# Performance work log

Hardware: AMD Instinct MI355X
Metric: run time of the kernel (lower is better)

Reference implementation:

```python
import jax, jax.numpy as jnp
from jax import lax
import numpy as np

LATENT = 64
NUM_LAYERS = 16
HIDDEN = 16
BATCH = 262144
NEG_SLOPE = 0.01


def setup_inputs() -> dict:
    key = jax.random.key(0)
    ks = jax.random.split(key, 9)
    scale = 0.1
    return {
        "x": jax.random.normal(ks[0], (BATCH, LATENT), dtype=jnp.float32),
        "sW1": scale * jax.random.normal(ks[1], (NUM_LAYERS, HIDDEN, LATENT), dtype=jnp.float32),
        "sb1": scale * jax.random.normal(ks[2], (NUM_LAYERS, HIDDEN), dtype=jnp.float32),
        "sW2": scale * jax.random.normal(ks[3], (NUM_LAYERS, LATENT, HIDDEN), dtype=jnp.float32),
        "sb2": scale * jax.random.normal(ks[4], (NUM_LAYERS, LATENT), dtype=jnp.float32),
        "tW1": scale * jax.random.normal(ks[5], (NUM_LAYERS, HIDDEN, LATENT), dtype=jnp.float32),
        "tb1": scale * jax.random.normal(ks[6], (NUM_LAYERS, HIDDEN), dtype=jnp.float32),
        "tW2": scale * jax.random.normal(ks[7], (NUM_LAYERS, LATENT, HIDDEN), dtype=jnp.float32),
        "tb2": scale * jax.random.normal(ks[8], (NUM_LAYERS, LATENT), dtype=jnp.float32),
    }


def _realnvp_forward(x, sW1, sb1, sW2, sb2, tW1, tb1, tW2, tb2):
    L, d = sW1.shape[0], x.shape[-1]
    # b[i] = 1 - i % 2  -> 1 on even indices; even layers use b, odd layers use 1-b
    base = (jnp.arange(d) % 2 == 0).astype(x.dtype)
    layer_even = (jnp.arange(L) % 2 == 0)[:, None]
    masks = jnp.where(layer_even, base[None, :], 1.0 - base[None, :])  # [L, d]

    def step(carry, p):
        z, ld = carry
        W1s, b1s, W2s, b2s, W1t, b1t, W2t, b2t, m = p
        zm = z * m  # [B, d]
        # s-net: Linear -> LeakyReLU(0.01) -> Linear -> Tanh
        hs = jax.nn.leaky_relu(zm @ W1s.T + b1s, NEG_SLOPE)
        scale = jnp.tanh(hs @ W2s.T + b2s)
        # t-net: Linear -> LeakyReLU(0.01) -> Linear
        ht = jax.nn.leaky_relu(zm @ W1t.T + b1t, NEG_SLOPE)
        trans = ht @ W2t.T + b2t
        # MaskedAffineFlow: z' = b*z + (1-b)*(z*exp(s) + t)
        z = zm + (1.0 - m) * (z * jnp.exp(scale) + trans)
        ld = ld + jnp.sum((1.0 - m) * scale, axis=-1)
        return (z, ld), None

    init = (x, jnp.zeros(x.shape[0], dtype=x.dtype))
    (z, ld), _ = lax.scan(step, init, (sW1, sb1, sW2, sb2, tW1, tb1, tW2, tb2, masks))
    return z[..., None], ld


def reference(x, sW1, sb1, sW2, sb2, tW1, tb1, tW2, tb2):
    return _realnvp_forward(x, sW1, sb1, sW2, sb2, tW1, tb1, tW2, tb2)
```

## Files before the change

kernel.cpp:

```cpp
#include <hip/hip_runtime.h>
#include <hip/hip_bf16.h>

#define NL 16
#define HID 16
#define LAT 64
#define BATCHN 262144

typedef __attribute__((ext_vector_type(4))) float f32x4;
typedef __attribute__((ext_vector_type(8))) short b16x8;

__device__ __forceinline__ f32x4 MFMA32(b16x8 a, b16x8 b, f32x4 c) {
  return __builtin_amdgcn_mfma_f32_16x16x32_bf16(a, b, c, 0, 0, 0);
}

__device__ __forceinline__ unsigned pk2(float lo, float hi) {
  __hip_bfloat162 h2 = __float22bfloat162_rn(float2{lo, hi});
  union { __hip_bfloat162 h; unsigned u; } u; u.h = h2; return u.u;
}

#if __has_builtin(__builtin_amdgcn_exp2f)
__device__ __forceinline__ float fexp2(float x) { return __builtin_amdgcn_exp2f(x); }
#else
__device__ __forceinline__ float fexp2(float x) { return __expf(0.6931471805599453f * x); }
#endif
#if __has_builtin(__builtin_amdgcn_rcpf)
__device__ __forceinline__ float frcp(float x) { return __builtin_amdgcn_rcpf(x); }
#else
__device__ __forceinline__ float frcp(float x) { return __fdividef(1.f, x); }
#endif

__device__ __forceinline__ short bfs(float f) {
  union { __hip_bfloat16 h; short s; } u; u.h = __float2bfloat16(f); return u.s;
}
__device__ __forceinline__ float leaky(float v) { return fmaxf(v, 0.01f * v); }
#define TWO_LOG2E 2.885390081777927f
#define LOG2E     1.442695040888963f

__global__ void prep_frags(
    const float* __restrict__ sW1, const float* __restrict__ sb1,
    const float* __restrict__ sW2, const float* __restrict__ sb2,
    const float* __restrict__ tW1, const float* __restrict__ tb1,
    const float* __restrict__ tW2, const float* __restrict__ tb2,
    b16x8* __restrict__ A1S, b16x8* __restrict__ A1T,
    b16x8* __restrict__ A2S, b16x8* __restrict__ A2T,
    f32x4* __restrict__ B1S, f32x4* __restrict__ B1T,
    f32x4* __restrict__ C2S, f32x4* __restrict__ C2T)
{
  const int l = blockIdx.x;
  const int lane = threadIdx.x;
  const int c = lane & 15, g = lane >> 4;
  const int PR = l & 1, PW = 1 - PR;
  const int idx = l * 64 + lane;

  b16x8 a;
  const float* w = sW1 + (l * HID + c) * LAT;
#pragma unroll
  for (int u = 0; u < 8; ++u) a[u] = bfs(w[16 * g + 2 * u + PR]);
  A1S[idx] = a;
  w = tW1 + (l * HID + c) * LAT;
#pragma unroll
  for (int u = 0; u < 8; ++u) a[u] = bfs(w[16 * g + 2 * u + PR]);
  A1T[idx] = a;
  B1S[idx] = ((const f32x4*)(sb1 + l * HID))[g];
  B1T[idx] = ((const f32x4*)(tb1 + l * HID))[g];

#pragma unroll
  for (int to = 0; to < 2; ++to) {
    const int m = 8 * (c >> 2) + 4 * to + (c & 3);
    const int d = 2 * m + PW;
    const int i2 = (l * 2 + to) * 64 + lane;
    b16x8 as = {0, 0, 0, 0, 0, 0, 0, 0}, at = {0, 0, 0, 0, 0, 0, 0, 0};
    const float* w2 = sW2 + (l * LAT + d) * HID + 4 * g;
#pragma unroll
    for (int j = 0; j < 4; ++j) as[j] = bfs(w2[j]);
    w2 = tW2 + (l * LAT + d) * HID + 4 * g;
#pragma unroll
    for (int j = 0; j < 4; ++j) at[4 + j] = bfs(w2[j]);
    A2S[i2] = as;
    A2T[i2] = at;
    f32x4 cs, ct;
#pragma unroll
    for (int j = 0; j < 4; ++j) {
      cs[j] = sb2[l * LAT + 16 * g + 8 * to + 2 * j + PW];
      ct[j] = tb2[l * LAT + 16 * g + 8 * to + 2 * j + PW];
    }
    C2S[i2] = cs;
    C2T[i2] = ct;
  }
}

template<int PR>
__device__ __forceinline__ void layer_step(
    b16x8 a1s, b16x8 a1t, b16x8 a2s0, b16x8 a2s1, b16x8 a2t0, b16x8 a2t1,
    f32x4 b1sv, f32x4 b1tv, f32x4 c2s0, f32x4 c2s1, f32x4 c2t0, f32x4 c2t1,
    f32x4 (&zst)[2][2][2], b16x8 (&zbf)[2][2], float (&rsum)[2][2])
{
  constexpr int PW = 1 - PR;
#pragma unroll
  for (int T = 0; T < 2; ++T) {
    const f32x4 hs = MFMA32(a1s, zbf[T][PR], b1sv);
    const f32x4 ht = MFMA32(a1t, zbf[T][PR], b1tv);
    union { unsigned u[4]; b16x8 v; } hc;
    hc.u[0] = pk2(leaky(hs[0]), leaky(hs[1]));
    hc.u[1] = pk2(leaky(hs[2]), leaky(hs[3]));
    hc.u[2] = pk2(leaky(ht[0]), leaky(ht[1]));
    hc.u[3] = pk2(leaky(ht[2]), leaky(ht[3]));
    const f32x4 ds0 = MFMA32(a2s0, hc.v, c2s0);
    const f32x4 dt0 = MFMA32(a2t0, hc.v, c2t0);
    const f32x4 ds1 = MFMA32(a2s1, hc.v, c2s1);
    const f32x4 dt1 = MFMA32(a2t1, hc.v, c2t1);
    f32x4 z0 = zst[T][PW][0], z1 = zst[T][PW][1];
#pragma unroll
    for (int j = 0; j < 4; ++j) {
      const float w0 = fexp2(TWO_LOG2E * ds0[j]);
      const float r0 = frcp(w0 + 1.f);
      rsum[T][0] += r0;
      z0[j] = fmaf(z0[j], fexp2(fmaf(-TWO_LOG2E, r0, LOG2E)), dt0[j]);
      const float w1 = fexp2(TWO_LOG2E * ds1[j]);
      const float r1 = frcp(w1 + 1.f);
      rsum[T][1] += r1;
      z1[j] = fmaf(z1[j], fexp2(fmaf(-TWO_LOG2E, r1, LOG2E)), dt1[j]);
    }
    zst[T][PW][0] = z0;
    zst[T][PW][1] = z1;
    union { unsigned u[4]; b16x8 v; } nz;
    nz.u[0] = pk2(z0[0], z0[1]);
    nz.u[1] = pk2(z0[2], z0[3]);
    nz.u[2] = pk2(z1[0], z1[1]);
    nz.u[3] = pk2(z1[2], z1[3]);
    zbf[T][PW] = nz.v;
  }
}

__global__ __launch_bounds__(256) void realnvp_fwd(
    const float* __restrict__ x, float* __restrict__ out,
    const b16x8* __restrict__ A1S, const b16x8* __restrict__ A1T,
    const b16x8* __restrict__ A2S, const b16x8* __restrict__ A2T,
    const f32x4* __restrict__ B1S, const f32x4* __restrict__ B1T,
    const f32x4* __restrict__ C2S, const f32x4* __restrict__ C2T)
{
  const int lane = threadIdx.x & 63;
  const int wv = threadIdx.x >> 6;
  const int c = lane & 15, g = lane >> 4;
  const int rowbase = (blockIdx.x * 4 + wv) * 32;

  f32x4 zst[2][2][2];
  b16x8 zbf[2][2];
  float rsum[2][2] = {{0.f, 0.f}, {0.f, 0.f}};
#pragma unroll
  for (int T = 0; T < 2; ++T) {
    const f32x4* xr = (const f32x4*)(x + (size_t)(rowbase + T * 16 + c) * LAT);
    const f32x4 q0 = xr[4 * g], q1 = xr[4 * g + 1], q2 = xr[4 * g + 2], q3 = xr[4 * g + 3];
    zst[T][0][0] = (f32x4){q0[0], q0[2], q1[0], q1[2]};
    zst[T][1][0] = (f32x4){q0[1], q0[3], q1[1], q1[3]};
    zst[T][0][1] = (f32x4){q2[0], q2[2], q3[0], q3[2]};
    zst[T][1][1] = (f32x4){q2[1], q2[3], q3[1], q3[3]};
#pragma unroll
    for (int p = 0; p < 2; ++p) {
      union { unsigned u[4]; b16x8 v; } zb;
      zb.u[0] = pk2(zst[T][p][0][0], zst[T][p][0][1]);
      zb.u[1] = pk2(zst[T][p][0][2], zst[T][p][0][3]);
      zb.u[2] = pk2(zst[T][p][1][0], zst[T][p][1][1]);
      zb.u[3] = pk2(zst[T][p][1][2], zst[T][p][1][3]);
      zbf[T][p] = zb.v;
    }
  }

#pragma unroll 2
  for (int lp = 0; lp < NL / 2; ++lp) {
    {
      const int i1 = (2 * lp) * 64 + lane, i2 = (4 * lp) * 64 + lane;
      layer_step<0>(A1S[i1], A1T[i1], A2S[i2], A2S[i2 + 64], A2T[i2], A2T[i2 + 64],
                    B1S[i1], B1T[i1], C2S[i2], C2S[i2 + 64], C2T[i2], C2T[i2 + 64],
                    zst, zbf, rsum);
    }
    {
      const int i1 = (2 * lp + 1) * 64 + lane, i2 = (4 * lp + 2) * 64 + lane;
      layer_step<1>(A1S[i1], A1T[i1], A2S[i2], A2S[i2 + 64], A2T[i2], A2T[i2 + 64],
                    B1S[i1], B1T[i1], C2S[i2], C2S[i2 + 64], C2T[i2], C2T[i2 + 64],
                    zst, zbf, rsum);
    }
  }

#pragma unroll
  for (int T = 0; T < 2; ++T) {
    f32x4* zo = (f32x4*)(out + (size_t)(rowbase + T * 16 + c) * LAT);
    const f32x4 e0 = zst[T][0][0], o0 = zst[T][1][0];
    const f32x4 e1 = zst[T][0][1], o1 = zst[T][1][1];
    zo[4 * g]     = (f32x4){e0[0], o0[0], e0[1], o0[1]};
    zo[4 * g + 1] = (f32x4){e0[2], o0[2], e0[3], o0[3]};
    zo[4 * g + 2] = (f32x4){e1[0], o1[0], e1[1], o1[1]};
    zo[4 * g + 3] = (f32x4){e1[2], o1[2], e1[3], o1[3]};
  }
  float ldv[2];
#pragma unroll
  for (int T = 0; T < 2; ++T) {
    float rs = rsum[T][0] + rsum[T][1];
    rs += __shfl_xor(rs, 16, 64);
    rs += __shfl_xor(rs, 32, 64);
    ldv[T] = fmaf(-2.f, rs, 512.f);
  }
  if (g < 2)
    out[(size_t)BATCHN * LAT + rowbase + g * 16 + c] = g ? ldv[1] : ldv[0];
}

extern "C" void kernel_launch(void* const* d_in, const int* in_sizes, int n_in,
                              void* d_out, int out_size, void* d_ws, size_t ws_size,
                              hipStream_t stream) {
  const float* x   = (const float*)d_in[0];
  const float* sW1 = (const float*)d_in[1];
  const float* sb1 = (const float*)d_in[2];
  const float* sW2 = (const float*)d_in[3];
  const float* sb2 = (const float*)d_in[4];
  const float* tW1 = (const float*)d_in[5];
  const float* tb1 = (const float*)d_in[6];
  const float* tW2 = (const float*)d_in[7];
  const float* tb2 = (const float*)d_in[8];
  float* out = (float*)d_out;

  char* w = (char*)d_ws;
  b16x8* A1S = (b16x8*)w;            w += NL * 64 * sizeof(b16x8);
  b16x8* A1T = (b16x8*)w;            w += NL * 64 * sizeof(b16x8);
  b16x8* A2S = (b16x8*)w;            w += NL * 128 * sizeof(b16x8);
  b16x8* A2T = (b16x8*)w;            w += NL * 128 * sizeof(b16x8);
  f32x4* B1S = (f32x4*)w;            w += NL * 64 * sizeof(f32x4);
  f32x4* B1T = (f32x4*)w;            w += NL * 64 * sizeof(f32x4);
  f32x4* C2S = (f32x4*)w;            w += NL * 128 * sizeof(f32x4);
  f32x4* C2T = (f32x4*)w;            w += NL * 128 * sizeof(f32x4);

  hipLaunchKernelGGL(prep_frags, dim3(NL), dim3(64), 0, stream,
                     sW1, sb1, sW2, sb2, tW1, tb1, tW2, tb2,
                     A1S, A1T, A2S, A2T, B1S, B1T, C2S, C2T);
  hipLaunchKernelGGL(realnvp_fwd, dim3(BATCHN / 128), dim3(256), 0, stream,
                     x, out, A1S, A1T, A2S, A2T, B1S, B1T, C2S, C2T);
}
```

Measured before the change: 105.1 us.

## Interleave per-layer weight fragments, fold tanh scale into weights, batch reciprocals

Prep now writes all fragments for one layer into a contiguous 12 KB block with a single base pointer, and pre-multiplies the s-net second layer weights and bias by 2*log2e so the exp2 argument needs no scaling. The tanh step replaces four reciprocals with one shared reciprocal of the product of four terms, with a clamp to avoid overflow. The main kernel moves to 64-thread blocks, one wave each, and the layer loop is no longer unrolled. This cuts transcendental and address work, at the cost of extra multiplies, possible precision loss from the product reciprocal, and four times as many blocks.

New measurement: 114.7 us. 1.09x slower.

```diff
diff --git a/kernel.cpp b/kernel.cpp
--- a/kernel.cpp
+++ b/kernel.cpp
@@ -5,6 +5,7 @@
 #define HID 16
 #define LAT 64
 #define BATCHN 262144
+#define LSTRIDE 12288
 
 typedef __attribute__((ext_vector_type(4))) float f32x4;
 typedef __attribute__((ext_vector_type(8))) short b16x8;
@@ -41,65 +42,75 @@
     const float* __restrict__ sW2, const float* __restrict__ sb2,
     const float* __restrict__ tW1, const float* __restrict__ tb1,
     const float* __restrict__ tW2, const float* __restrict__ tb2,
-    b16x8* __restrict__ A1S, b16x8* __restrict__ A1T,
-    b16x8* __restrict__ A2S, b16x8* __restrict__ A2T,
-    f32x4* __restrict__ B1S, f32x4* __restrict__ B1T,
-    f32x4* __restrict__ C2S, f32x4* __restrict__ C2T)
+    char* __restrict__ ws)
 {
   const int l = blockIdx.x;
   const int lane = threadIdx.x;
   const int c = lane & 15, g = lane >> 4;
   const int PR = l & 1, PW = 1 - PR;
-  const int idx = l * 64 + lane;
+  char* base = ws + (size_t)l * LSTRIDE + lane * 16;
 
   b16x8 a;
   const float* w = sW1 + (l * HID + c) * LAT;
 #pragma unroll
   for (int u = 0; u < 8; ++u) a[u] = bfs(w[16 * g + 2 * u + PR]);
-  A1S[idx] = a;
+  *(b16x8*)(base) = a;
   w = tW1 + (l * HID + c) * LAT;
 #pragma unroll
   for (int u = 0; u < 8; ++u) a[u] = bfs(w[16 * g + 2 * u + PR]);
-  A1T[idx] = a;
-  B1S[idx] = ((const f32x4*)(sb1 + l * HID))[g];
-  B1T[idx] = ((const f32x4*)(tb1 + l * HID))[g];
+  *(b16x8*)(base + 1024) = a;
+  *(f32x4*)(base + 2048) = ((const f32x4*)(sb1 + l * HID))[g];
+  *(f32x4*)(base + 3072) = ((const f32x4*)(tb1 + l * HID))[g];
 
 #pragma unroll
   for (int to = 0; to < 2; ++to) {
     const int m = 8 * (c >> 2) + 4 * to + (c & 3);
     const int d = 2 * m + PW;
-    const int i2 = (l * 2 + to) * 64 + lane;
     b16x8 as = {0, 0, 0, 0, 0, 0, 0, 0}, at = {0, 0, 0, 0, 0, 0, 0, 0};
     const float* w2 = sW2 + (l * LAT + d) * HID + 4 * g;
 #pragma unroll
-    for (int j = 0; j < 4; ++j) as[j] = bfs(w2[j]);
+    for (int j = 0; j < 4; ++j) as[j] = bfs(TWO_LOG2E * w2[j]);
     w2 = tW2 + (l * LAT + d) * HID + 4 * g;
 #pragma unroll
     for (int j = 0; j < 4; ++j) at[4 + j] = bfs(w2[j]);
-    A2S[i2] = as;
-    A2T[i2] = at;
+    *(b16x8*)(base + 4096 + to * 1024) = as;
+    *(b16x8*)(base + 6144 + to * 1024) = at;
     f32x4 cs, ct;
 #pragma unroll
     for (int j = 0; j < 4; ++j) {
-      cs[j] = sb2[l * LAT + 16 * g + 8 * to + 2 * j + PW];
+      cs[j] = TWO_LOG2E * sb2[l * LAT + 16 * g + 8 * to + 2 * j + PW];
       ct[j] = tb2[l * LAT + 16 * g + 8 * to + 2 * j + PW];
     }
-    C2S[i2] = cs;
-    C2T[i2] = ct;
+    *(f32x4*)(base + 8192 + to * 1024) = cs;
+    *(f32x4*)(base + 10240 + to * 1024) = ct;
   }
 }
 
 template<int PR>
 __device__ __forceinline__ void layer_step(
-    b16x8 a1s, b16x8 a1t, b16x8 a2s0, b16x8 a2s1, b16x8 a2t0, b16x8 a2t1,
-    f32x4 b1sv, f32x4 b1tv, f32x4 c2s0, f32x4 c2s1, f32x4 c2t0, f32x4 c2t1,
+    const char* __restrict__ b0,
     f32x4 (&zst)[2][2][2], b16x8 (&zbf)[2][2], float (&rsum)[2][2])
 {
   constexpr int PW = 1 - PR;
-#pragma unroll
-  for (int T = 0; T < 2; ++T) {
-    const f32x4 hs = MFMA32(a1s, zbf[T][PR], b1sv);
-    const f32x4 ht = MFMA32(a1t, zbf[T][PR], b1tv);
+  const char* b1 = b0 + 4096;
+  const char* b2 = b0 + 8192;
+  const b16x8 a1s  = *(const b16x8*)(b0);
+  const b16x8 a1t  = *(const b16x8*)(b0 + 1024);
+  const f32x4 b1s  = *(const f32x4*)(b0 + 2048);
+  const f32x4 b1t  = *(const f32x4*)(b0 + 3072);
+  const b16x8 a2s0 = *(const b16x8*)(b1);
+  const b16x8 a2s1 = *(const b16x8*)(b1 + 1024);
+  const b16x8 a2t0 = *(const b16x8*)(b1 + 2048);
+  const b16x8 a2t1 = *(const b16x8*)(b1 + 3072);
+  const f32x4 c2s0 = *(const f32x4*)(b2);
+  const f32x4 c2s1 = *(const f32x4*)(b2 + 1024);
+  const f32x4 c2t0 = *(const f32x4*)(b2 + 2048);
+  const f32x4 c2t1 = *(const f32x4*)(b2 + 3072);
+
+#pragma unroll
+  for (int T = 0; T < 2; ++T) {
+    const f32x4 hs = MFMA32(a1s, zbf[T][PR], b1s);
+    const f32x4 ht = MFMA32(a1t, zbf[T][PR], b1t);
     union { unsigned u[4]; b16x8 v; } hc;
     hc.u[0] = pk2(leaky(hs[0]), leaky(hs[1]));
     hc.u[1] = pk2(leaky(hs[2]), leaky(hs[3]));
@@ -110,16 +121,28 @@
     const f32x4 ds1 = MFMA32(a2s1, hc.v, c2s1);
     const f32x4 dt1 = MFMA32(a2t1, hc.v, c2t1);
     f32x4 z0 = zst[T][PW][0], z1 = zst[T][PW][1];
+
+    f32x4 a0v, a1v;
 #pragma unroll
     for (int j = 0; j < 4; ++j) {
-      const float w0 = fexp2(TWO_LOG2E * ds0[j]);
-      const float r0 = frcp(w0 + 1.f);
-      rsum[T][0] += r0;
-      z0[j] = fmaf(z0[j], fexp2(fmaf(-TWO_LOG2E, r0, LOG2E)), dt0[j]);
-      const float w1 = fexp2(TWO_LOG2E * ds1[j]);
-      const float r1 = frcp(w1 + 1.f);
-      rsum[T][1] += r1;
-      z1[j] = fmaf(z1[j], fexp2(fmaf(-TWO_LOG2E, r1, LOG2E)), dt1[j]);
+      a0v[j] = fexp2(fminf(ds0[j], 25.f)) + 1.f;
+      a1v[j] = fexp2(fminf(ds1[j], 25.f)) + 1.f;
+    }
+    const float m01a = a0v[0] * a0v[1], m23a = a0v[2] * a0v[3];
+    const float Ra = frcp(m01a * m23a);
+    const float R01a = Ra * m23a, R23a = Ra * m01a;
+    const f32x4 r0v = {R01a * a0v[1], R01a * a0v[0], R23a * a0v[3], R23a * a0v[2]};
+    const float m01b = a1v[0] * a1v[1], m23b = a1v[2] * a1v[3];
+    const float Rb = frcp(m01b * m23b);
+    const float R01b = Rb * m23b, R23b = Rb * m01b;
+    const f32x4 r1v = {R01b * a1v[1], R01b * a1v[0], R23b * a1v[3], R23b * a1v[2]};
+
+#pragma unroll
+    for (int j = 0; j < 4; ++j) {
+      rsum[T][0] += r0v[j];
+      z0[j] = fmaf(z0[j], fexp2(fmaf(-TWO_LOG2E, r0v[j], LOG2E)), dt0[j]);
+      rsum[T][1] += r1v[j];
+      z1[j] = fmaf(z1[j], fexp2(fmaf(-TWO_LOG2E, r1v[j], LOG2E)), dt1[j]);
     }
     zst[T][PW][0] = z0;
     zst[T][PW][1] = z1;
@@ -132,17 +155,13 @@
   }
 }
 
-__global__ __launch_bounds__(256) void realnvp_fwd(
+__global__ __launch_bounds__(64) void realnvp_fwd(
     const float* __restrict__ x, float* __restrict__ out,
-    const b16x8* __restrict__ A1S, const b16x8* __restrict__ A1T,
-    const b16x8* __restrict__ A2S, const b16x8* __restrict__ A2T,
-    const f32x4* __restrict__ B1S, const f32x4* __restrict__ B1T,
-    const f32x4* __restrict__ C2S, const f32x4* __restrict__ C2T)
+    const char* __restrict__ ws)
 {
-  const int lane = threadIdx.x & 63;
-  const int wv = threadIdx.x >> 6;
+  const int lane = threadIdx.x;
   const int c = lane & 15, g = lane >> 4;
-  const int rowbase = (blockIdx.x * 4 + wv) * 32;
+  const int rowbase = blockIdx.x * 32;
 
   f32x4 zst[2][2][2];
   b16x8 zbf[2][2];
@@ -166,20 +185,12 @@
     }
   }
 
-#pragma unroll 2
+  const char* b0 = ws + lane * 16;
+#pragma unroll 1
   for (int lp = 0; lp < NL / 2; ++lp) {
-    {
-      const int i1 = (2 * lp) * 64 + lane, i2 = (4 * lp) * 64 + lane;
-      layer_step<0>(A1S[i1], A1T[i1], A2S[i2], A2S[i2 + 64], A2T[i2], A2T[i2 + 64],
-                    B1S[i1], B1T[i1], C2S[i2], C2S[i2 + 64], C2T[i2], C2T[i2 + 64],
-                    zst, zbf, rsum);
-    }
-    {
-      const int i1 = (2 * lp + 1) * 64 + lane, i2 = (4 * lp + 2) * 64 + lane;
-      layer_step<1>(A1S[i1], A1T[i1], A2S[i2], A2S[i2 + 64], A2T[i2], A2T[i2 + 64],
-                    B1S[i1], B1T[i1], C2S[i2], C2S[i2 + 64], C2T[i2], C2T[i2 + 64],
-                    zst, zbf, rsum);
-    }
+    layer_step<0>(b0, zst, zbf, rsum);
+    layer_step<1>(b0 + LSTRIDE, zst, zbf, rsum);
+    b0 += 2 * LSTRIDE;
   }
 
 #pragma unroll
@@ -217,20 +228,10 @@
   const float* tW2 = (const float*)d_in[7];
   const float* tb2 = (const float*)d_in[8];
   float* out = (float*)d_out;
-
-  char* w = (char*)d_ws;
-  b16x8* A1S = (b16x8*)w;            w += NL * 64 * sizeof(b16x8);
-  b16x8* A1T = (b16x8*)w;            w += NL * 64 * sizeof(b16x8);
-  b16x8* A2S = (b16x8*)w;            w += NL * 128 * sizeof(b16x8);
-  b16x8* A2T = (b16x8*)w;            w += NL * 128 * sizeof(b16x8);
-  f32x4* B1S = (f32x4*)w;            w += NL * 64 * sizeof(f32x4);
-  f32x4* B1T = (f32x4*)w;            w += NL * 64 * sizeof(f32x4);
-  f32x4* C2S = (f32x4*)w;            w += NL * 128 * sizeof(f32x4);
-  f32x4* C2T = (f32x4*)w;            w += NL * 128 * sizeof(f32x4);
+  char* ws = (char*)d_ws;
 
   hipLaunchKernelGGL(prep_frags, dim3(NL), dim3(64), 0, stream,
-                     sW1, sb1, sW2, sb2, tW1, tb1, tW2, tb2,
-                     A1S, A1T, A2S, A2T, B1S, B1T, C2S, C2T);
-  hipLaunchKernelGGL(realnvp_fwd, dim3(BATCHN / 128), dim3(256), 0, stream,
-                     x, out, A1S, A1T, A2S, A2T, B1S, B1T, C2S, C2T);
-}
+                     sW1, sb1, sW2, sb2, tW1, tb1, tW2, tb2, ws);
+  hipLaunchKernelGGL(realnvp_fwd, dim3(BATCHN / 32), dim3(64), 0, stream,
+                     x, out, ws);
+}
```
